# Performance work log

Hardware: AMD Instinct MI355X
Metric: run time of the kernel (lower is better)

The kernel has to match this reference:

```python
import jax, jax.numpy as jnp
import numpy as np

D_MODEL = 1024
NHEAD = 16
SPARSITY = 0.9  # keep prob = 1 - sparsity
NEG = -1e30    # stand-in for -inf; avoids NaN on (rare) fully-masked rows
EPS = 1e-5


def _layernorm(x, g, b):
    mu = jnp.mean(x, axis=-1, keepdims=True)
    var = jnp.mean(jnp.square(x - mu), axis=-1, keepdims=True)
    return (x - mu) * jax.lax.rsqrt(var + EPS) * g + b


def setup_inputs() -> dict:
    key = jax.random.key(0)
    ks = jax.random.split(key, 12)
    B, S, D = 2, 2048, D_MODEL
    H = NHEAD
    s = 1.0 / np.sqrt(D)
    inp = {
        "x": jax.random.normal(ks[0], (B, S, D), jnp.float32),
        # torch: torch.rand((B,H,S,S)) > sparsity, resampled each forward
        "mask": jax.random.uniform(ks[1], (B, H, S, S), jnp.float32) > SPARSITY,
        "Wq": jax.random.normal(ks[2], (D, D), jnp.float32) * s,
        "bq": jnp.zeros((D,), jnp.float32),
        "Wk": jax.random.normal(ks[3], (D, D), jnp.float32) * s,
        "bk": jnp.zeros((D,), jnp.float32),
        "Wv": jax.random.normal(ks[4], (D, D), jnp.float32) * s,
        "bv": jnp.zeros((D,), jnp.float32),
        "Wo": jax.random.normal(ks[5], (D, D), jnp.float32) * s,
        "bo": jnp.zeros((D,), jnp.float32),
        "ln1_g": jnp.ones((D,), jnp.float32),
        "ln1_b": jnp.zeros((D,), jnp.float32),
        "ln2_g": jnp.ones((D,), jnp.float32),
        "ln2_b": jnp.zeros((D,), jnp.float32),
        "W1": jax.random.normal(ks[6], (D, 4 * D), jnp.float32) * s,
        "b1f": jnp.zeros((4 * D,), jnp.float32),
        "W2": jax.random.normal(ks[7], (4 * D, D), jnp.float32) * (1.0 / np.sqrt(4 * D)),
        "b2f": jnp.zeros((D,), jnp.float32),
    }
    return inp


def reference(x, mask, Wq, bq, Wk, bk, Wv, bv, Wo, bo,
              ln1_g, ln1_b, ln2_g, ln2_b, W1, b1f, W2, b2f):
    B, S, D = x.shape
    H = NHEAD
    dk = D // H
    # projections -> (B, H, S, dk)
    q = (x @ Wq + bq).reshape(B, S, H, dk).transpose(0, 2, 1, 3)
    k = (x @ Wk + bk).reshape(B, S, H, dk).transpose(0, 2, 1, 3)
    v = (x @ Wv + bv).reshape(B, S, H, dk).transpose(0, 2, 1, 3)
    scores = jnp.einsum('bhqd,bhkd->bhqk', q, k) / np.sqrt(dk)
    scores = jnp.where(mask, scores, NEG)
    attn = jax.nn.softmax(scores, axis=-1)
    ctx = jnp.einsum('bhqk,bhkd->bhqd', attn, v)          # (B,H,S,dk)
    ctx = ctx.transpose(0, 2, 1, 3).reshape(B, S, D)
    attn_out = ctx @ Wo + bo
    x = _layernorm(x + attn_out, ln1_g, ln1_b)
    ff = jax.nn.relu(x @ W1 + b1f) @ W2 + b2f             # eval: dropout off
    return _layernorm(x + ff, ln2_g, ln2_b)
```

## Files before the change

kernel.cpp:

```cpp
#include <hip/hip_runtime.h>
#include <stdint.h>


typedef __attribute__((ext_vector_type(8))) short short8;
typedef __attribute__((ext_vector_type(4))) float f32x4;
typedef __attribute__((ext_vector_type(4))) unsigned short u16x4;

__device__ __forceinline__ unsigned short f2bf(float f) {
    union { float f; unsigned u; } v; v.f = f;
    unsigned r = v.u + 0x7fffu + ((v.u >> 16) & 1u);
    return (unsigned short)(r >> 16);
}

__device__ __forceinline__ void gload16(const void* gsrc, void* ldst) {
    __builtin_amdgcn_global_load_lds(
        (const __attribute__((address_space(1))) void*)gsrc,
        (__attribute__((address_space(3))) void*)ldst,
        16, 0, 0);
}

__global__ __launch_bounds__(256) void f32_to_bf16_k(
    const float* __restrict__ in, unsigned short* __restrict__ out, int n4)
{
    int i = blockIdx.x * 256 + threadIdx.x;
    if (i < n4) {
        f32x4 v = *(const f32x4*)&in[(size_t)i * 4];
        u16x4 o = { f2bf(v[0]), f2bf(v[1]), f2bf(v[2]), f2bf(v[3]) };
        *(u16x4*)&out[(size_t)i * 4] = o;
    }
}

__global__ __launch_bounds__(256) void transpose_k(
    const float* __restrict__ W, unsigned short* __restrict__ Wt, int K, int N)
{
    __shared__ float tile[32][33];
    const int n0 = blockIdx.x * 32, k0 = blockIdx.y * 32;
    const int tx = threadIdx.x & 31, ty = threadIdx.x >> 5;
#pragma unroll
    for (int i = 0; i < 32; i += 8)
        tile[ty + i][tx] = W[(size_t)(k0 + ty + i) * N + n0 + tx];
    __syncthreads();
#pragma unroll
    for (int i = 0; i < 32; i += 8)
        Wt[(size_t)(n0 + ty + i) * K + k0 + tx] = f2bf(tile[tx][ty + i]);
}

__global__ __launch_bounds__(256) void vtrans_k(
    const unsigned short* __restrict__ qkv, unsigned short* __restrict__ vt)
{
    __shared__ unsigned short tile[32][34];
    const int s0 = blockIdx.x * 32;
    const int d0 = blockIdx.y * 32;
    const int bh = blockIdx.z, b = bh >> 4, h = bh & 15;
    const int tx = threadIdx.x & 31, ty = threadIdx.x >> 5;
#pragma unroll
    for (int i = 0; i < 32; i += 8)
        tile[ty + i][tx] = qkv[(size_t)(b * 2048 + s0 + ty + i) * 3072 + 2048 + h * 64 + d0 + tx];
    __syncthreads();
#pragma unroll
    for (int i = 0; i < 32; i += 8)
        vt[((size_t)bh * 64 + d0 + ty + i) * 2048 + s0 + tx] = tile[tx][ty + i];
}

__global__ void concat3_k(const float* a, const float* b, const float* c, float* out)
{
    int i = blockIdx.x * 256 + threadIdx.x;
    if (i < 3072) out[i] = (i < 1024) ? a[i] : (i < 2048 ? b[i - 1024] : c[i - 2048]);
}

__global__ __launch_bounds__(1024) void detect_mask_k(
    const unsigned int* __restrict__ m, int* __restrict__ flag)
{
    __shared__ int f1, f2;
    if (threadIdx.x == 0) { f1 = 0; f2 = 0; }
    __syncthreads();
    int l1 = 0, l2 = 0;
    for (int i = threadIdx.x; i < 65536; i += 1024) {
        unsigned v = m[i];
        l1 |= (v > 1u);
        l2 |= (v != 0u && v != 0x3f800000u);
    }
    if (l1) atomicOr(&f1, 1);
    if (l2) atomicOr(&f2, 1);
    __syncthreads();
    if (threadIdx.x == 0) {
        int mode = 0;
        if (f1) mode = f2 ? 1 : 2;
        *flag = mode;
    }
}

__global__ __launch_bounds__(256) void pack_mask_k(
    const void* __restrict__ mask, const int* __restrict__ flag,
    unsigned long long* __restrict__ packed, long long nelem)
{
    const int mode = *flag;
    const long long stride = (long long)gridDim.x * 256;
    long long i = (long long)blockIdx.x * 256 + threadIdx.x;
    if (mode == 0) {
        const int* m = (const int*)mask;
        for (; i < nelem; i += stride) {
            unsigned long long bl = __ballot(m[i] != 0);
            if ((threadIdx.x & 63) == 0) packed[i >> 6] = bl;
        }
    } else if (mode == 1) {
        const unsigned char* m = (const unsigned char*)mask;
        for (; i < nelem; i += stride) {
            unsigned long long bl = __ballot(m[i] != 0);
            if ((threadIdx.x & 63) == 0) packed[i >> 6] = bl;
        }
    } else {
        const float* m = (const float*)mask;
        for (; i < nelem; i += stride) {
            unsigned long long bl = __ballot(m[i] != 0.f);
            if ((threadIdx.x & 63) == 0) packed[i >> 6] = bl;
        }
    }
}

template<int EPI>
__global__ __launch_bounds__(256) void gemm_bt(
    const unsigned short* __restrict__ A, const unsigned short* __restrict__ Bt,
    const float* __restrict__ bias, const float* __restrict__ resid,
    void* __restrict__ Cout, int M, int N, int K)
{
    __shared__ unsigned short As[128 * 64];
    __shared__ unsigned short Bs[128 * 64];
    const int t = threadIdx.x;
    const int lane = t & 63, wid = t >> 6;
    const int l16 = lane & 15, g = lane >> 4;
    const int wr = wid >> 1, wc = wid & 1;
    const int bm = blockIdx.y * 128, bn = blockIdx.x * 128;

    f32x4 acc[4][4] = {};

    for (int k0 = 0; k0 < K; k0 += 64) {
        __syncthreads();
#pragma unroll
        for (int i = 0; i < 4; ++i) {
            int linear = i * 2048 + t * 8;
            int row = linear >> 6, col = linear & 63;
            gload16(&A[(size_t)(bm + row) * K + k0 + col], &As[linear]);
        }
#pragma unroll
        for (int i = 0; i < 4; ++i) {
            int linear = i * 2048 + t * 8;
            int row = linear >> 6, col = linear & 63;
            gload16(&Bt[(size_t)(bn + row) * K + k0 + col], &Bs[linear]);
        }
        __syncthreads();
#pragma unroll
        for (int kc = 0; kc < 2; ++kc) {
            short8 a[4], b[4];
#pragma unroll
            for (int m = 0; m < 4; ++m)
                a[m] = *(const short8*)&As[(wr * 64 + m * 16 + l16) * 64 + kc * 32 + g * 8];
#pragma unroll
            for (int n = 0; n < 4; ++n)
                b[n] = *(const short8*)&Bs[(wc * 64 + n * 16 + l16) * 64 + kc * 32 + g * 8];
#pragma unroll
            for (int m = 0; m < 4; ++m)
#pragma unroll
                for (int n = 0; n < 4; ++n)
                    acc[m][n] = __builtin_amdgcn_mfma_f32_16x16x32_bf16(a[m], b[n], acc[m][n], 0, 0, 0);
        }
    }

#pragma unroll
    for (int m = 0; m < 4; ++m) {
        const int row0 = bm + wr * 64 + m * 16 + g * 4;
#pragma unroll
        for (int n = 0; n < 4; ++n) {
            const int col = bn + wc * 64 + n * 16 + l16;
            const float bb = bias[col];
#pragma unroll
            for (int r = 0; r < 4; ++r) {
                float v = acc[m][n][r] + bb;
                const size_t idx = (size_t)(row0 + r) * N + col;
                if (EPI == 2) {
                    ((float*)Cout)[idx] = v + resid[idx];
                } else {
                    if (EPI == 1) v = fmaxf(v, 0.f);
                    ((unsigned short*)Cout)[idx] = f2bf(v);
                }
            }
        }
    }
}

__global__ __launch_bounds__(256) void attn_k(
    const unsigned short* __restrict__ qkv,
    const unsigned short* __restrict__ vt,
    const unsigned long long* __restrict__ pmask,
    unsigned short* __restrict__ ctx)
{
    __shared__ unsigned short Pl[4][16 * 72];
    const int t = threadIdx.x, lane = t & 63, w = t >> 6;
    const int l16 = lane & 15, g = lane >> 4;
    const int bh = blockIdx.y;
    const int b = bh >> 4, h = bh & 15;
    const int q0 = blockIdx.x * 64;

    const size_t rowQ = (size_t)(b * 2048 + q0 + w * 16 + l16) * 3072 + h * 64;
    const short8 qf0 = *(const short8*)&qkv[rowQ + g * 8];
    const short8 qf1 = *(const short8*)&qkv[rowQ + 32 + g * 8];

    const unsigned long long* mbase =
        pmask + ((size_t)bh * 2048 + q0 + w * 16 + g * 4) * 32;
    const unsigned short* vbase = &vt[(size_t)bh * 64 * 2048];

    f32x4 acc[4] = {};
    float mrow[4], lrow[4];
#pragma unroll
    for (int j = 0; j < 4; ++j) { mrow[j] = -INFINITY; lrow[j] = 0.f; }

    for (int kt = 0; kt < 32; ++kt) {
        unsigned long long mw[4];
#pragma unroll
        for (int j = 0; j < 4; ++j) mw[j] = mbase[j * 32 + kt];

        f32x4 s[4] = {};
#pragma unroll
        for (int n = 0; n < 4; ++n) {
            const size_t rowK = (size_t)(b * 2048 + kt * 64 + n * 16 + l16) * 3072 + 1024 + h * 64;
            const short8 kf0 = *(const short8*)&qkv[rowK + g * 8];
            const short8 kf1 = *(const short8*)&qkv[rowK + 32 + g * 8];
            s[n] = __builtin_amdgcn_mfma_f32_16x16x32_bf16(qf0, kf0, s[n], 0, 0, 0);
            s[n] = __builtin_amdgcn_mfma_f32_16x16x32_bf16(qf1, kf1, s[n], 0, 0, 0);
        }

#pragma unroll
        for (int n = 0; n < 4; ++n) {
            const int sh = n * 16 + l16;
#pragma unroll
            for (int j = 0; j < 4; ++j) {
                const bool keep = (mw[j] >> sh) & 1ull;
                s[n][j] = keep ? s[n][j] * 0.125f : -1e30f;
            }
        }

#pragma unroll
        for (int j = 0; j < 4; ++j) {
            float mx = fmaxf(fmaxf(s[0][j], s[1][j]), fmaxf(s[2][j], s[3][j]));
#pragma unroll
            for (int d = 1; d < 16; d <<= 1) mx = fmaxf(mx, __shfl_xor(mx, d));
            const float mn = fmaxf(mrow[j], mx);
            float p0 = __expf(s[0][j] - mn), p1 = __expf(s[1][j] - mn);
            float p2 = __expf(s[2][j] - mn), p3 = __expf(s[3][j] - mn);
            s[0][j] = p0; s[1][j] = p1; s[2][j] = p2; s[3][j] = p3;
            float sm = p0 + p1 + p2 + p3;
#pragma unroll
            for (int d = 1; d < 16; d <<= 1) sm += __shfl_xor(sm, d);
            const float scale = __expf(mrow[j] - mn);
            lrow[j] = lrow[j] * scale + sm;
            mrow[j] = mn;
#pragma unroll
            for (int n = 0; n < 4; ++n) acc[n][j] *= scale;
        }

#pragma unroll
        for (int n = 0; n < 4; ++n)
#pragma unroll
            for (int j = 0; j < 4; ++j)
                Pl[w][(g * 4 + j) * 72 + n * 16 + l16] = f2bf(s[n][j]);

#pragma unroll
        for (int c = 0; c < 2; ++c) {
            const short8 pf = *(const short8*)&Pl[w][l16 * 72 + c * 32 + g * 8];
#pragma unroll
            for (int n = 0; n < 4; ++n) {
                const short8 vf = *(const short8*)&vbase[(size_t)(n * 16 + l16) * 2048 + kt * 64 + c * 32 + g * 8];
                acc[n] = __builtin_amdgcn_mfma_f32_16x16x32_bf16(pf, vf, acc[n], 0, 0, 0);
            }
        }
    }

#pragma unroll
    for (int n = 0; n < 4; ++n)
#pragma unroll
        for (int j = 0; j < 4; ++j) {
            const int q = q0 + w * 16 + g * 4 + j;
            ctx[(size_t)(b * 2048 + q) * 1024 + h * 64 + n * 16 + l16] = f2bf(acc[n][j] / lrow[j]);
        }
}

template<int WB>
__global__ __launch_bounds__(256) void ln_k(
    const float* __restrict__ in, const float* __restrict__ gw, const float* __restrict__ bw,
    float* __restrict__ outF, unsigned short* __restrict__ outB)
{
    __shared__ float red[2][4];
    const int row = blockIdx.x, t = threadIdx.x;
    const f32x4 v = *(const f32x4*)&in[(size_t)row * 1024 + t * 4];
    float s = v[0] + v[1] + v[2] + v[3];
    float ss = v[0] * v[0] + v[1] * v[1] + v[2] * v[2] + v[3] * v[3];
#pragma unroll
    for (int d = 1; d < 64; d <<= 1) { s += __shfl_xor(s, d); ss += __shfl_xor(ss, d); }
    if ((t & 63) == 0) { red[0][t >> 6] = s; red[1][t >> 6] = ss; }
    __syncthreads();
    s = red[0][0] + red[0][1] + red[0][2] + red[0][3];
    ss = red[1][0] + red[1][1] + red[1][2] + red[1][3];
    const float mu = s * (1.f / 1024.f);
    const float var = ss * (1.f / 1024.f) - mu * mu;
    const float rs = rsqrtf(var + 1e-5f);
    f32x4 y;
#pragma unroll
    for (int e = 0; e < 4; ++e)
        y[e] = (v[e] - mu) * rs * gw[t * 4 + e] + bw[t * 4 + e];
    *(f32x4*)&outF[(size_t)row * 1024 + t * 4] = y;
    if (WB) {
        u16x4 o = { f2bf(y[0]), f2bf(y[1]), f2bf(y[2]), f2bf(y[3]) };
        *(u16x4*)&outB[(size_t)row * 1024 + t * 4] = o;
    }
}

extern "C" void kernel_launch(void* const* d_in, const int* in_sizes, int n_in,
                              void* d_out, int out_size, void* d_ws, size_t ws_size,
                              hipStream_t stream)
{
    (void)n_in; (void)out_size; (void)ws_size;
    const float* x   = (const float*)d_in[0];
    const void*  mask = d_in[1];
    const float* Wq  = (const float*)d_in[2];
    const float* bq  = (const float*)d_in[3];
    const float* Wk  = (const float*)d_in[4];
    const float* bk  = (const float*)d_in[5];
    const float* Wv  = (const float*)d_in[6];
    const float* bv  = (const float*)d_in[7];
    const float* Wo  = (const float*)d_in[8];
    const float* bo  = (const float*)d_in[9];
    const float* g1  = (const float*)d_in[10];
    const float* be1 = (const float*)d_in[11];
    const float* g2  = (const float*)d_in[12];
    const float* be2 = (const float*)d_in[13];
    const float* W1  = (const float*)d_in[14];
    const float* b1  = (const float*)d_in[15];
    const float* W2  = (const float*)d_in[16];
    const float* b2  = (const float*)d_in[17];

    const int M = 4096;
    const long long maskN = in_sizes[1];

    char* wsb = (char*)d_ws;
    size_t off = 0;
    auto alloc = [&](size_t bytes) -> char* {
        char* p = wsb + off;
        off += (bytes + 255) & ~(size_t)255;
        return p;
    };
    int*            flag   = (int*)           alloc(256);
    unsigned long long* pm = (unsigned long long*)alloc((size_t)(maskN / 64) * 8);
    unsigned short* xb     = (unsigned short*)alloc((size_t)M * 1024 * 2);
    unsigned short* wqkvT  = (unsigned short*)alloc((size_t)3072 * 1024 * 2);
    unsigned short* woT    = (unsigned short*)alloc((size_t)1024 * 1024 * 2);
    unsigned short* w1T    = (unsigned short*)alloc((size_t)4096 * 1024 * 2);
    unsigned short* w2T    = (unsigned short*)alloc((size_t)1024 * 4096 * 2);
    float*          bqkv   = (float*)         alloc(3072 * 4);
    unsigned short* qkv    = (unsigned short*)alloc((size_t)M * 3072 * 2);
    unsigned short* vtb    = (unsigned short*)alloc((size_t)32 * 64 * 2048 * 2);
    unsigned short* ctxb   = (unsigned short*)alloc((size_t)M * 1024 * 2);
    float*          r1f    = (float*)         alloc((size_t)M * 1024 * 4);
    float*          x1f    = (float*)         alloc((size_t)M * 1024 * 4);
    unsigned short* x1b    = (unsigned short*)alloc((size_t)M * 1024 * 2);
    unsigned short* hb     = (unsigned short*)alloc((size_t)M * 4096 * 2);

    detect_mask_k<<<1, 1024, 0, stream>>>((const unsigned int*)mask, flag);
    pack_mask_k<<<2048, 256, 0, stream>>>(mask, flag, pm, maskN);
    f32_to_bf16_k<<<4096, 256, 0, stream>>>(x, xb, M * 1024 / 4);
    transpose_k<<<dim3(32, 32),  256, 0, stream>>>(Wq, wqkvT,                1024, 1024);
    transpose_k<<<dim3(32, 32),  256, 0, stream>>>(Wk, wqkvT + 1024 * 1024,  1024, 1024);
    transpose_k<<<dim3(32, 32),  256, 0, stream>>>(Wv, wqkvT + 2048 * 1024,  1024, 1024);
    transpose_k<<<dim3(32, 32),  256, 0, stream>>>(Wo, woT,                  1024, 1024);
    transpose_k<<<dim3(128, 32), 256, 0, stream>>>(W1, w1T, 1024, 4096);
    transpose_k<<<dim3(32, 128), 256, 0, stream>>>(W2, w2T, 4096, 1024);
    concat3_k<<<12, 256, 0, stream>>>(bq, bk, bv, bqkv);

    gemm_bt<0><<<dim3(24, 32), 256, 0, stream>>>(xb, wqkvT, bqkv, nullptr, qkv, M, 3072, 1024);
    vtrans_k<<<dim3(64, 2, 32), 256, 0, stream>>>(qkv, vtb);
    attn_k<<<dim3(32, 32), 256, 0, stream>>>(qkv, vtb, pm, ctxb);
    gemm_bt<2><<<dim3(8, 32), 256, 0, stream>>>(ctxb, woT, bo, x, r1f, M, 1024, 1024);
    ln_k<1><<<4096, 256, 0, stream>>>(r1f, g1, be1, x1f, x1b);
    gemm_bt<1><<<dim3(32, 32), 256, 0, stream>>>(x1b, w1T, b1, nullptr, hb, M, 4096, 1024);
    gemm_bt<2><<<dim3(8, 32), 256, 0, stream>>>(hb, w2T, b2, x1f, r1f, M, 1024, 4096);
    ln_k<0><<<4096, 256, 0, stream>>>(r1f, g2, be2, (float*)d_out, nullptr);
}
```

Before: 1.315 ms.

## Add 256x256 ping-pong pipelined GEMM for QKV and FFN1 projections

Introduces a 512-thread GEMM kernel with 256x256 output tiles, double-buffered swizzled LDS filled by direct global-to-LDS loads, and an eight-phase schedule that interleaves staging of the next K tiles with MFMA work. It also remaps workgroups across the XCDs. The QKV and FFN1 GEMMs switch to it to get more data reuse per tile and overlap memory with compute. In exchange it uses more registers and LDS, launches fewer workgroups (192 and 256), and depends on fragile barrier and vmcnt ordering.

Measured after the change: 1.295 ms. About the same (-1.5%).

```diff
diff --git a/kernel.cpp b/kernel.cpp
--- a/kernel.cpp
+++ b/kernel.cpp
@@ -18,6 +18,8 @@
         (__attribute__((address_space(3))) void*)ldst,
         16, 0, 0);
 }
+
+__device__ __forceinline__ int SWZ(int b) { return b ^ (((b >> 9) & 1) << 5); }
 
 __global__ __launch_bounds__(256) void f32_to_bf16_k(
     const float* __restrict__ in, unsigned short* __restrict__ out, int n4)
@@ -114,6 +116,121 @@
         for (; i < nelem; i += stride) {
             unsigned long long bl = __ballot(m[i] != 0.f);
             if ((threadIdx.x & 63) == 0) packed[i >> 6] = bl;
+        }
+    }
+}
+
+template<int EPI>
+__global__ __launch_bounds__(512) void gemm256_bt(
+    const unsigned short* __restrict__ A, const unsigned short* __restrict__ Bt,
+    const float* __restrict__ bias, void* __restrict__ Cout,
+    int M, int N, int K)
+{
+    __shared__ __align__(16) unsigned short lds[2][2][256 * 64];
+    const int t = threadIdx.x;
+    const int lane = t & 63;
+    const int wid = t >> 6;
+    const int l16 = lane & 15, g = lane >> 4;
+    const int wr = wid >> 2, wc = wid & 3;
+
+    const int nbx = gridDim.x, nwg = nbx * gridDim.y;
+    const int orig = blockIdx.y * nbx + blockIdx.x;
+    const int qq = nwg >> 3, rr = nwg & 7;
+    const int xcd = orig & 7, idx = orig >> 3;
+    const int wg = (xcd < rr) ? (xcd * (qq + 1) + idx)
+                              : (rr * (qq + 1) + (xcd - rr) * qq + idx);
+    const int bm = (wg / nbx) * 256, bn = (wg % nbx) * 256;
+
+    const int ntiles = K >> 6;
+    auto kof = [&](int s) { return (s < ntiles ? s : ntiles - 1) << 6; };
+
+    auto stage_half = [&](const unsigned short* __restrict__ P, int grow0, int k0,
+                          int buf, int ab, int half) {
+#pragma unroll
+        for (int rnd = 0; rnd < 2; ++rnd) {
+            const int off = rnd * 8192 + t * 16;
+            const int sw  = SWZ(off);
+            const int row = off >> 7;
+            const int col = (sw & 127) >> 1;
+            gload16(&P[(size_t)(grow0 + half * 128 + row) * K + k0 + col],
+                    &lds[buf][ab][half * 8192 + (off >> 1)]);
+        }
+    };
+
+    auto lda = [&](int buf, int m, int kc) -> short8 {
+        const int byte = ((m * 32 + wr * 16 + l16) * 64 + kc * 32 + g * 8) * 2;
+        return *(const short8*)((const char*)&lds[buf][0][0] + SWZ(byte));
+    };
+    auto ldb = [&](int buf, int n, int kc) -> short8 {
+        const int byte = ((n * 64 + wc * 16 + l16) * 64 + kc * 32 + g * 8) * 2;
+        return *(const short8*)((const char*)&lds[buf][1][0] + SWZ(byte));
+    };
+
+    f32x4 acc[8][4] = {};
+    short8 af[4][2];
+
+    stage_half(A,  bm, 0,  0, 0, 0);
+    stage_half(A,  bm, 0,  0, 0, 1);
+    stage_half(Bt, bn, 0,  0, 1, 0);
+    stage_half(Bt, bn, 0,  0, 1, 1);
+    stage_half(A,  bm, 64, 1, 0, 0);
+    stage_half(Bt, bn, 64, 1, 1, 0);
+    asm volatile("s_waitcnt vmcnt(4)" ::: "memory");
+    __builtin_amdgcn_s_barrier();
+
+#define PH(buf, mh, nh, doLoadA, STAGE_STMT, doVM)                                  \
+  {                                                                                  \
+    if (doLoadA) {                                                                   \
+      _Pragma("unroll") for (int mm = 0; mm < 4; ++mm)                               \
+      _Pragma("unroll") for (int kc = 0; kc < 2; ++kc)                               \
+        af[mm][kc] = lda(buf, (mh) * 4 + mm, kc);                                    \
+    }                                                                                \
+    short8 bf[2][2];                                                                 \
+    _Pragma("unroll") for (int nn = 0; nn < 2; ++nn)                                 \
+    _Pragma("unroll") for (int kc = 0; kc < 2; ++kc)                                 \
+      bf[nn][kc] = ldb(buf, (nh) * 2 + nn, kc);                                      \
+    STAGE_STMT;                                                                      \
+    __builtin_amdgcn_s_barrier();                                                    \
+    __builtin_amdgcn_s_setprio(1);                                                   \
+    _Pragma("unroll") for (int mm = 0; mm < 4; ++mm)                                 \
+    _Pragma("unroll") for (int nn = 0; nn < 2; ++nn)                                 \
+    _Pragma("unroll") for (int kc = 0; kc < 2; ++kc)                                 \
+      acc[(mh) * 4 + mm][(nh) * 2 + nn] = __builtin_amdgcn_mfma_f32_16x16x32_bf16(   \
+          af[mm][kc], bf[nn][kc], acc[(mh) * 4 + mm][(nh) * 2 + nn], 0, 0, 0);       \
+    __builtin_amdgcn_s_setprio(0);                                                   \
+    if (doVM) { asm volatile("s_waitcnt vmcnt(4)" ::: "memory"); }                   \
+    __builtin_amdgcn_s_barrier();                                                    \
+  }
+
+    const int half_ntiles = ntiles >> 1;
+    for (int i = 0; i < half_ntiles; ++i) {
+        const int k1 = (2 * i + 1) << 6;
+        const int k2 = kof(2 * i + 2);
+        const int k3 = kof(2 * i + 3);
+        PH(0, 0, 0, 1, (stage_half(A,  bm, k1, 1, 0, 1)), 0)
+        PH(0, 0, 1, 0, (stage_half(Bt, bn, k1, 1, 1, 1)), 0)
+        PH(0, 1, 0, 1, (stage_half(A,  bm, k2, 0, 0, 0)), 0)
+        PH(0, 1, 1, 0, (stage_half(Bt, bn, k2, 0, 1, 0)), 1)
+        PH(1, 0, 0, 1, (stage_half(A,  bm, k2, 0, 0, 1)), 0)
+        PH(1, 0, 1, 0, (stage_half(Bt, bn, k2, 0, 1, 1)), 0)
+        PH(1, 1, 0, 1, (stage_half(A,  bm, k3, 1, 0, 0)), 0)
+        PH(1, 1, 1, 0, (stage_half(Bt, bn, k3, 1, 1, 0)), 1)
+    }
+#undef PH
+
+#pragma unroll
+    for (int m = 0; m < 8; ++m) {
+        const int row0 = bm + m * 32 + wr * 16 + g * 4;
+#pragma unroll
+        for (int n = 0; n < 4; ++n) {
+            const int col = bn + n * 64 + wc * 16 + l16;
+            const float bb = bias[col];
+#pragma unroll
+            for (int r = 0; r < 4; ++r) {
+                float v = acc[m][n][r] + bb;
+                if (EPI == 1) v = fmaxf(v, 0.f);
+                ((unsigned short*)Cout)[(size_t)(row0 + r) * N + col] = f2bf(v);
+            }
         }
     }
 }
@@ -375,12 +492,12 @@
     transpose_k<<<dim3(32, 128), 256, 0, stream>>>(W2, w2T, 4096, 1024);
     concat3_k<<<12, 256, 0, stream>>>(bq, bk, bv, bqkv);
 
-    gemm_bt<0><<<dim3(24, 32), 256, 0, stream>>>(xb, wqkvT, bqkv, nullptr, qkv, M, 3072, 1024);
+    gemm256_bt<0><<<dim3(12, 16), 512, 0, stream>>>(xb, wqkvT, bqkv, qkv, M, 3072, 1024);
     vtrans_k<<<dim3(64, 2, 32), 256, 0, stream>>>(qkv, vtb);
     attn_k<<<dim3(32, 32), 256, 0, stream>>>(qkv, vtb, pm, ctxb);
     gemm_bt<2><<<dim3(8, 32), 256, 0, stream>>>(ctxb, woT, bo, x, r1f, M, 1024, 1024);
     ln_k<1><<<4096, 256, 0, stream>>>(r1f, g1, be1, x1f, x1b);
-    gemm_bt<1><<<dim3(32, 32), 256, 0, stream>>>(x1b, w1T, b1, nullptr, hb, M, 4096, 1024);
+    gemm256_bt<1><<<dim3(16, 16), 512, 0, stream>>>(x1b, w1T, b1, hb, M, 4096, 1024);
     gemm_bt<2><<<dim3(8, 32), 256, 0, stream>>>(hb, w2T, b2, x1f, r1f, M, 1024, 4096);
     ln_k<0><<<4096, 256, 0, stream>>>(r1f, g2, be2, (float*)d_out, nullptr);
 }
```
